# Kernel tuning notes

Measured on AMD Instinct MI355X. Metric: run time of the kernel, lower is better.

Reference implementation:

```python
import jax, jax.numpy as jnp
import numpy as np

N = 50000
D = 128
C = 40
E = 600000


def gcn_conv(x, src, dst, W, b, n):
    # PyG GCNConv: h = x @ W^T; symmetric deg^-1/2 normalization over
    # edges (self-loops already appended in src/dst); bias added after agg.
    h = x @ W.T                                   # [N, D_out]
    deg = jnp.zeros((n,), h.dtype).at[dst].add(jnp.ones((src.shape[0],), h.dtype))
    dinv = jnp.where(deg > 0, jax.lax.rsqrt(deg), 0.0)
    norm = dinv[src] * dinv[dst]                  # [E+N]
    msg = h[src] * norm[:, None]                  # gather + scale
    out = jnp.zeros_like(h).at[dst].add(msg)      # scatter-add aggregation
    return out + b


def setup_inputs() -> dict:
    key = jax.random.key(0)
    ks = jax.random.split(key, 8)
    x = jax.random.normal(ks[0], (N, D), dtype=jnp.float32)
    edge_index = jax.random.randint(ks[1], (2, E), 0, N, dtype=jnp.int64)
    s = 1.0 / np.sqrt(D)
    W1 = jax.random.uniform(ks[2], (D, D), jnp.float32, -s, s)
    b1 = jnp.zeros((D,), jnp.float32)
    W2 = jax.random.uniform(ks[3], (D, D), jnp.float32, -s, s)
    b2 = jnp.zeros((D,), jnp.float32)
    Wl = jax.random.uniform(ks[4], (C, D), jnp.float32, -s, s)
    bl = jnp.zeros((C,), jnp.float32)
    return {"x": x, "edge_index": edge_index, "W1": W1, "b1": b1,
            "W2": W2, "b2": b2, "Wl": Wl, "bl": bl}


def reference(x, edge_index, W1, b1, W2, b2, Wl, bl):
    n = x.shape[0]
    loop = jnp.arange(n, dtype=edge_index.dtype)
    src = jnp.concatenate([edge_index[0], loop])  # add self-loops
    dst = jnp.concatenate([edge_index[1], loop])
    h = gcn_conv(x, src, dst, W1, b1, n)
    h = jax.nn.relu(h)  # dropout is identity in eval mode
    h = gcn_conv(h, src, dst, W2, b2, n)
    h = jax.nn.relu(h)
    logits = h @ Wl.T + bl
    return jax.nn.log_softmax(logits, axis=1)
```

## Files before the change

### kernel.cpp

```cpp
#include <hip/hip_runtime.h>
#include <math.h>

#define FD  128
#define CAP 64

static __device__ __forceinline__ float4 ld4(const float* p){ return *(const float4*)p; }


__global__ __launch_bounds__(256) void k_fill(const int* __restrict__ src, const int* __restrict__ dst,
                                              int* __restrict__ cnt, int* __restrict__ bcol, int e){
    int i = blockIdx.x*blockDim.x + threadIdx.x;
    if (i < e){
        int s = src[i], d = dst[i];
        int pos = atomicAdd(&cnt[d], 1);
        if (pos < CAP) bcol[d*CAP + pos] = s;
    }
}


__global__ __launch_bounds__(256, 2) void k_gemm(const float* __restrict__ A, const float* __restrict__ W,
                                                 float* __restrict__ out, int nrows,
                                                 int* __restrict__ zcnt, int zn)
{
    __shared__ float Wt[128*128];
    __shared__ float xs[32*128];
    const int tid  = threadIdx.x;
    const int row0 = blockIdx.x * 32;

    int gid = blockIdx.x*256 + tid;
    if (zcnt && gid < zn) zcnt[gid] = 0;

    #pragma unroll
    for (int it = 0; it < 16; ++it){
        int idx4 = it*256 + tid;
        int j  = idx4 & 127;
        int k0 = (idx4 >> 7) << 2;
        float4 w = ld4(W + j*FD + k0);
        int jg = j >> 2, je = j & 3;
        Wt[(k0+0)*128 + (((jg + 2*(k0+0)) & 31) << 2) + je] = w.x;
        Wt[(k0+1)*128 + (((jg + 2*(k0+1)) & 31) << 2) + je] = w.y;
        Wt[(k0+2)*128 + (((jg + 2*(k0+2)) & 31) << 2) + je] = w.z;
        Wt[(k0+3)*128 + (((jg + 2*(k0+3)) & 31) << 2) + je] = w.w;
    }
    #pragma unroll
    for (int it = 0; it < 4; ++it){
        int idx4 = it*256 + tid;
        int r  = idx4 >> 5;
        int kq = idx4 & 31;
        int row = row0 + r;
        float4 v = make_float4(0.f,0.f,0.f,0.f);
        if (row < nrows) v = ld4(A + (size_t)row*FD + kq*4);
        *(float4*)&xs[r*128 + (((kq + r) & 31) << 2)] = v;
    }
    __syncthreads();

    const int tr = tid >> 4;
    const int tc = tid & 15;
    float acc[2][2][4];
    #pragma unroll
    for (int i = 0; i < 2; ++i)
        #pragma unroll
        for (int hh = 0; hh < 2; ++hh)
            #pragma unroll
            for (int u = 0; u < 4; ++u) acc[i][hh][u] = 0.f;

    #pragma unroll 4
    for (int k0 = 0; k0 < 128; k0 += 4){
        int kq = k0 >> 2;
        float4 a0 = *(const float4*)&xs[(2*tr+0)*128 + (((kq + 2*tr+0) & 31) << 2)];
        float4 a1 = *(const float4*)&xs[(2*tr+1)*128 + (((kq + 2*tr+1) & 31) << 2)];
        #pragma unroll
        for (int kk = 0; kk < 4; ++kk){
            int k = k0 + kk;
            float4 w0 = *(const float4*)&Wt[k*128 + (((tc      + 2*k) & 31) << 2)];
            float4 w1 = *(const float4*)&Wt[k*128 + (((tc + 16 + 2*k) & 31) << 2)];
            float av0 = (kk==0)?a0.x:(kk==1)?a0.y:(kk==2)?a0.z:a0.w;
            float av1 = (kk==0)?a1.x:(kk==1)?a1.y:(kk==2)?a1.z:a1.w;
            acc[0][0][0] += av0*w0.x; acc[0][0][1] += av0*w0.y; acc[0][0][2] += av0*w0.z; acc[0][0][3] += av0*w0.w;
            acc[0][1][0] += av0*w1.x; acc[0][1][1] += av0*w1.y; acc[0][1][2] += av0*w1.z; acc[0][1][3] += av0*w1.w;
            acc[1][0][0] += av1*w0.x; acc[1][0][1] += av1*w0.y; acc[1][0][2] += av1*w0.z; acc[1][0][3] += av1*w0.w;
            acc[1][1][0] += av1*w1.x; acc[1][1][1] += av1*w1.y; acc[1][1][2] += av1*w1.z; acc[1][1][3] += av1*w1.w;
        }
    }

    #pragma unroll
    for (int i = 0; i < 2; ++i){
        int row = row0 + 2*tr + i;
        if (row < nrows){
            *(float4*)(out + (size_t)row*FD + 4*tc)      = make_float4(acc[i][0][0],acc[i][0][1],acc[i][0][2],acc[i][0][3]);
            *(float4*)(out + (size_t)row*FD + 64 + 4*tc) = make_float4(acc[i][1][0],acc[i][1][1],acc[i][1][2],acc[i][1][3]);
        }
    }
}


__global__ __launch_bounds__(256) void k_agg(const float* __restrict__ t, const float* __restrict__ bias,
    const int* __restrict__ cnt, const int* __restrict__ bcol,
    float* __restrict__ out, int n, int relu)
{
    int node = (blockIdx.x*blockDim.x + threadIdx.x) >> 6;
    int lane = threadIdx.x & 63;
    if (node >= n) return;

    float2 b   = *(const float2*)(bias + lane*2);
    int deg = cnt[node];
    int dg  = min(deg, CAP);
    float dv = rsqrtf((float)(deg + 1));

    int   c_l = 0; float w_l = 0.f;
    if (lane < dg){
        c_l = bcol[node*CAP + lane];
        w_l = dv * rsqrtf((float)(cnt[c_l] + 1));
    }

    float2 acc = *(const float2*)(t + (size_t)node*FD + lane*2);
    float sw = dv*dv;
    acc.x = acc.x*sw + b.x;
    acc.y = acc.y*sw + b.y;

    int e = 0;
    for (; e + 4 <= dg; e += 4){
        int   c0 = __shfl(c_l, e,   64), c1 = __shfl(c_l, e+1, 64);
        int   c2 = __shfl(c_l, e+2, 64), c3 = __shfl(c_l, e+3, 64);
        float w0 = __shfl(w_l, e,   64), w1 = __shfl(w_l, e+1, 64);
        float w2 = __shfl(w_l, e+2, 64), w3 = __shfl(w_l, e+3, 64);
        float2 u0 = *(const float2*)(t + (size_t)c0*FD + lane*2);
        float2 u1 = *(const float2*)(t + (size_t)c1*FD + lane*2);
        float2 u2 = *(const float2*)(t + (size_t)c2*FD + lane*2);
        float2 u3 = *(const float2*)(t + (size_t)c3*FD + lane*2);
        acc.x += w0*u0.x + w1*u1.x + w2*u2.x + w3*u3.x;
        acc.y += w0*u0.y + w1*u1.y + w2*u2.y + w3*u3.y;
    }
    for (; e < dg; ++e){
        int   c = __shfl(c_l, e, 64);
        float w = __shfl(w_l, e, 64);
        float2 u = *(const float2*)(t + (size_t)c*FD + lane*2);
        acc.x += w*u.x; acc.y += w*u.y;
    }

    if (relu){ acc.x = fmaxf(acc.x, 0.f); acc.y = fmaxf(acc.y, 0.f); }
    *(float2*)(out + (size_t)node*FD + lane*2) = acc;
}


__global__ __launch_bounds__(320) void k_final(const float* __restrict__ h, const float* __restrict__ Wl,
    const float* __restrict__ bl, float* __restrict__ out, int n)
{
    __shared__ float Wt[128*41];
    __shared__ float xs[64*128];
    __shared__ float lg[64*41];
    const int tid  = threadIdx.x;
    const int row0 = blockIdx.x * 64;

    for (int idx4 = tid; idx4 < 1280; idx4 += 320){
        int j  = idx4 >> 5;
        int k0 = (idx4 & 31) << 2;
        float4 w = ld4(Wl + j*FD + k0);
        Wt[(k0+0)*41 + j] = w.x;
        Wt[(k0+1)*41 + j] = w.y;
        Wt[(k0+2)*41 + j] = w.z;
        Wt[(k0+3)*41 + j] = w.w;
    }
    for (int idx4 = tid; idx4 < 2048; idx4 += 320){
        int r = idx4 >> 5, kq = idx4 & 31;
        int row = row0 + r;
        float4 v = make_float4(0.f,0.f,0.f,0.f);
        if (row < n) v = ld4(h + (size_t)row*FD + kq*4);
        *(float4*)&xs[r*128 + kq*4] = v;
    }
    __syncthreads();

    const int c  = tid % 40;
    const int rb = tid / 40;
    float acc[8];
    #pragma unroll
    for (int i = 0; i < 8; ++i) acc[i] = 0.f;
    #pragma unroll 4
    for (int k = 0; k < 128; ++k){
        float w = Wt[k*41 + c];
        #pragma unroll
        for (int i = 0; i < 8; ++i) acc[i] += xs[(rb*8+i)*128 + k] * w;
    }
    float bv = bl[c];
    #pragma unroll
    for (int i = 0; i < 8; ++i) lg[(rb*8+i)*41 + c] = acc[i] + bv;
    __syncthreads();

    if (tid < 64){
        int row = row0 + tid;
        if (row < n){
            float v[40];
            #pragma unroll
            for (int j = 0; j < 40; ++j) v[j] = lg[tid*41 + j];
            float m = v[0];
            #pragma unroll
            for (int j = 1; j < 40; ++j) m = fmaxf(m, v[j]);
            float s = 0.f;
            #pragma unroll
            for (int j = 0; j < 40; ++j) s += expf(v[j] - m);
            float lse = m + logf(s);
            float* o = out + (size_t)row*40;
            #pragma unroll
            for (int j4 = 0; j4 < 10; ++j4){
                *(float4*)(o + 4*j4) = make_float4(v[4*j4+0]-lse, v[4*j4+1]-lse,
                                                   v[4*j4+2]-lse, v[4*j4+3]-lse);
            }
        }
    }
}


extern "C" void kernel_launch(void* const* d_in, const int* in_sizes, int n_in,
                              void* d_out, int out_size, void* d_ws, size_t ws_size,
                              hipStream_t stream)
{
    const float* x   = (const float*)d_in[0];
    const int*   ei  = (const int*)d_in[1];
    const float* W1  = (const float*)d_in[2];
    const float* b1  = (const float*)d_in[3];
    const float* W2  = (const float*)d_in[4];
    const float* b2  = (const float*)d_in[5];
    const float* Wl  = (const float*)d_in[6];
    const float* bl  = (const float*)d_in[7];
    float*       out = (float*)d_out;

    const int n = in_sizes[0] / FD;
    const int e = in_sizes[1] / 2;
    const int* src = ei;
    const int* dst = ei + e;

    char* p = (char*)d_ws;
    auto alloc = [&](size_t bytes)->char* {
        char* q = p; p += (bytes + 255) & ~(size_t)255; return q;
    };
    int*   cnt  = (int*)  alloc((size_t)n*4);
    int*   bcol = (int*)  alloc((size_t)n*CAP*4);
    float* t    = (float*)alloc((size_t)n*FD*4);
    float* h    = (float*)alloc((size_t)n*FD*4);

    const int gemm_grid  = (n + 31)/32;
    const int agg_grid   = (n + 3)/4;
    const int fill_grid  = (e + 255)/256;
    const int final_grid = (n + 63)/64;

    hipLaunchKernelGGL(k_gemm, dim3(gemm_grid), dim3(256), 0, stream, x, W1, t, n, cnt, n);
    hipLaunchKernelGGL(k_fill, dim3(fill_grid), dim3(256), 0, stream, src, dst, cnt, bcol, e);
    hipLaunchKernelGGL(k_agg,  dim3(agg_grid),  dim3(256), 0, stream, t, b1, cnt, bcol, h, n, 1);
    hipLaunchKernelGGL(k_gemm, dim3(gemm_grid), dim3(256), 0, stream, h, W2, t, n, (int*)nullptr, 0);
    hipLaunchKernelGGL(k_agg,  dim3(agg_grid),  dim3(256), 0, stream, t, b2, cnt, bcol, h, n, 1);
    hipLaunchKernelGGL(k_final, dim3(final_grid), dim3(320), 0, stream, h, Wl, bl, out, n);
}
```

Measured before the change: 329.7 us.

## Replace FP32 SIMT GEMM with split-bf16 MFMA GEMM and precomputed weight halves

Replaces the shared-memory FP32 FMA GEMM with a per-wave MFMA kernel using 16x16x32 bf16 instructions. Fp32 accuracy is approximated by splitting activations and weights into high and low bf16 parts and accumulating three products. A new prologue kernel converts W1/W2 to bf16 hi/lo arrays and zeroes the degree counters, which the old GEMM used to do. Weights are now read straight from global/L2 per wave rather than staged in LDS, and the output is written as scalar strided stores, which may cost memory efficiency; precision is slightly reduced versus pure fp32.

```diff
diff --git a/kernel.cpp b/kernel.cpp
--- a/kernel.cpp
+++ b/kernel.cpp
@@ -4,7 +4,39 @@
 #define FD  128
 #define CAP 64
 
+
 static __device__ __forceinline__ float4 ld4(const float* p){ return *(const float4*)p; }
+
+typedef __attribute__((ext_vector_type(8))) short bf16x8;
+typedef __attribute__((ext_vector_type(4))) float f32x4;
+
+static __device__ __forceinline__ unsigned short f2bf(float f){
+    union { float f; unsigned u; } c; c.f = f;
+    unsigned u = c.u + 0x7fffu + ((c.u >> 16) & 1u);
+    return (unsigned short)(u >> 16);
+}
+static __device__ __forceinline__ float bf2f(unsigned short b){
+    union { float f; unsigned u; } c; c.u = ((unsigned)b) << 16;
+    return c.f;
+}
+
+
+__global__ __launch_bounds__(256) void k_wconv(const float* __restrict__ W1, const float* __restrict__ W2,
+                                               unsigned short* __restrict__ w1h, unsigned short* __restrict__ w1l,
+                                               unsigned short* __restrict__ w2h, unsigned short* __restrict__ w2l,
+                                               int* __restrict__ cnt, int n)
+{
+    int i = blockIdx.x*256 + threadIdx.x;
+    if (i < n) cnt[i] = 0;
+    if (i < FD*FD){
+        float a = W1[i];
+        unsigned short ah = f2bf(a);
+        w1h[i] = ah; w1l[i] = f2bf(a - bf2f(ah));
+        float b = W2[i];
+        unsigned short bh = f2bf(b);
+        w2h[i] = bh; w2l[i] = f2bf(b - bf2f(bh));
+    }
+}
 
 
 __global__ __launch_bounds__(256) void k_fill(const int* __restrict__ src, const int* __restrict__ dst,
@@ -18,77 +50,64 @@
 }
 
 
-__global__ __launch_bounds__(256, 2) void k_gemm(const float* __restrict__ A, const float* __restrict__ W,
-                                                 float* __restrict__ out, int nrows,
-                                                 int* __restrict__ zcnt, int zn)
-{
-    __shared__ float Wt[128*128];
-    __shared__ float xs[32*128];
-    const int tid  = threadIdx.x;
-    const int row0 = blockIdx.x * 32;
-
-    int gid = blockIdx.x*256 + tid;
-    if (zcnt && gid < zn) zcnt[gid] = 0;
-
-    #pragma unroll
-    for (int it = 0; it < 16; ++it){
-        int idx4 = it*256 + tid;
-        int j  = idx4 & 127;
-        int k0 = (idx4 >> 7) << 2;
-        float4 w = ld4(W + j*FD + k0);
-        int jg = j >> 2, je = j & 3;
-        Wt[(k0+0)*128 + (((jg + 2*(k0+0)) & 31) << 2) + je] = w.x;
-        Wt[(k0+1)*128 + (((jg + 2*(k0+1)) & 31) << 2) + je] = w.y;
-        Wt[(k0+2)*128 + (((jg + 2*(k0+2)) & 31) << 2) + je] = w.z;
-        Wt[(k0+3)*128 + (((jg + 2*(k0+3)) & 31) << 2) + je] = w.w;
-    }
-    #pragma unroll
-    for (int it = 0; it < 4; ++it){
-        int idx4 = it*256 + tid;
-        int r  = idx4 >> 5;
-        int kq = idx4 & 31;
-        int row = row0 + r;
-        float4 v = make_float4(0.f,0.f,0.f,0.f);
-        if (row < nrows) v = ld4(A + (size_t)row*FD + kq*4);
-        *(float4*)&xs[r*128 + (((kq + r) & 31) << 2)] = v;
-    }
-    __syncthreads();
-
-    const int tr = tid >> 4;
-    const int tc = tid & 15;
-    float acc[2][2][4];
-    #pragma unroll
-    for (int i = 0; i < 2; ++i)
+__global__ __launch_bounds__(256) void k_gemm_mfma(const float* __restrict__ A,
+                                                   const unsigned short* __restrict__ Wh,
+                                                   const unsigned short* __restrict__ Wl,
+                                                   float* __restrict__ out, int nrows)
+{
+    const int lane = threadIdx.x & 63;
+    const int wid  = (blockIdx.x*blockDim.x + threadIdx.x) >> 6;
+    const int i0   = wid * 16;
+    if (i0 >= nrows) return;
+
+    const int mr = lane & 15;
+    const int kg = lane >> 4;
+
+    int arow = i0 + mr;
+    if (arow >= nrows) arow = nrows - 1;
+    const float* ap = A + (size_t)arow*FD + kg*8;
+
+    bf16x8 ahf[4], alf[4];
+    #pragma unroll
+    for (int kt = 0; kt < 4; ++kt){
+        float4 a0 = ld4(ap + 32*kt);
+        float4 a1 = ld4(ap + 32*kt + 4);
+        float v0 = a0.x, v1 = a0.y, v2 = a0.z, v3 = a0.w;
+        float v4 = a1.x, v5 = a1.y, v6 = a1.z, v7 = a1.w;
+        unsigned short h0=f2bf(v0),h1=f2bf(v1),h2=f2bf(v2),h3=f2bf(v3);
+        unsigned short h4=f2bf(v4),h5=f2bf(v5),h6=f2bf(v6),h7=f2bf(v7);
+        ahf[kt][0]=(short)h0; ahf[kt][1]=(short)h1; ahf[kt][2]=(short)h2; ahf[kt][3]=(short)h3;
+        ahf[kt][4]=(short)h4; ahf[kt][5]=(short)h5; ahf[kt][6]=(short)h6; ahf[kt][7]=(short)h7;
+        alf[kt][0]=(short)f2bf(v0-bf2f(h0)); alf[kt][1]=(short)f2bf(v1-bf2f(h1));
+        alf[kt][2]=(short)f2bf(v2-bf2f(h2)); alf[kt][3]=(short)f2bf(v3-bf2f(h3));
+        alf[kt][4]=(short)f2bf(v4-bf2f(h4)); alf[kt][5]=(short)f2bf(v5-bf2f(h5));
+        alf[kt][6]=(short)f2bf(v6-bf2f(h6)); alf[kt][7]=(short)f2bf(v7-bf2f(h7));
+    }
+
+    f32x4 acc[8];
+    #pragma unroll
+    for (int jt = 0; jt < 8; ++jt){ acc[jt][0]=0.f; acc[jt][1]=0.f; acc[jt][2]=0.f; acc[jt][3]=0.f; }
+
+    #pragma unroll
+    for (int kt = 0; kt < 4; ++kt){
         #pragma unroll
-        for (int hh = 0; hh < 2; ++hh)
-            #pragma unroll
-            for (int u = 0; u < 4; ++u) acc[i][hh][u] = 0.f;
-
-    #pragma unroll 4
-    for (int k0 = 0; k0 < 128; k0 += 4){
-        int kq = k0 >> 2;
-        float4 a0 = *(const float4*)&xs[(2*tr+0)*128 + (((kq + 2*tr+0) & 31) << 2)];
-        float4 a1 = *(const float4*)&xs[(2*tr+1)*128 + (((kq + 2*tr+1) & 31) << 2)];
-        #pragma unroll
-        for (int kk = 0; kk < 4; ++kk){
-            int k = k0 + kk;
-            float4 w0 = *(const float4*)&Wt[k*128 + (((tc      + 2*k) & 31) << 2)];
-            float4 w1 = *(const float4*)&Wt[k*128 + (((tc + 16 + 2*k) & 31) << 2)];
-            float av0 = (kk==0)?a0.x:(kk==1)?a0.y:(kk==2)?a0.z:a0.w;
-            float av1 = (kk==0)?a1.x:(kk==1)?a1.y:(kk==2)?a1.z:a1.w;
-            acc[0][0][0] += av0*w0.x; acc[0][0][1] += av0*w0.y; acc[0][0][2] += av0*w0.z; acc[0][0][3] += av0*w0.w;
-            acc[0][1][0] += av0*w1.x; acc[0][1][1] += av0*w1.y; acc[0][1][2] += av0*w1.z; acc[0][1][3] += av0*w1.w;
-            acc[1][0][0] += av1*w0.x; acc[1][0][1] += av1*w0.y; acc[1][0][2] += av1*w0.z; acc[1][0][3] += av1*w0.w;
-            acc[1][1][0] += av1*w1.x; acc[1][1][1] += av1*w1.y; acc[1][1][2] += av1*w1.z; acc[1][1][3] += av1*w1.w;
+        for (int jt = 0; jt < 8; ++jt){
+            size_t off = (size_t)(16*jt + mr)*FD + 32*kt + 8*kg;
+            bf16x8 wh = *(const bf16x8*)(Wh + off);
+            bf16x8 wl = *(const bf16x8*)(Wl + off);
+            acc[jt] = __builtin_amdgcn_mfma_f32_16x16x32_bf16(ahf[kt], wh, acc[jt], 0, 0, 0);
+            acc[jt] = __builtin_amdgcn_mfma_f32_16x16x32_bf16(ahf[kt], wl, acc[jt], 0, 0, 0);
+            acc[jt] = __builtin_amdgcn_mfma_f32_16x16x32_bf16(alf[kt], wh, acc[jt], 0, 0, 0);
         }
     }
 
     #pragma unroll
-    for (int i = 0; i < 2; ++i){
-        int row = row0 + 2*tr + i;
-        if (row < nrows){
-            *(float4*)(out + (size_t)row*FD + 4*tc)      = make_float4(acc[i][0][0],acc[i][0][1],acc[i][0][2],acc[i][0][3]);
-            *(float4*)(out + (size_t)row*FD + 64 + 4*tc) = make_float4(acc[i][1][0],acc[i][1][1],acc[i][1][2],acc[i][1][3]);
+    for (int r = 0; r < 4; ++r){
+        int orow = i0 + kg*4 + r;
+        if (orow < nrows){
+            float* op = out + (size_t)orow*FD + mr;
+            #pragma unroll
+            for (int jt = 0; jt < 8; ++jt) op[16*jt] = acc[jt][r];
         }
     }
 }
@@ -233,20 +252,29 @@
     auto alloc = [&](size_t bytes)->char* {
         char* q = p; p += (bytes + 255) & ~(size_t)255; return q;
     };
-    int*   cnt  = (int*)  alloc((size_t)n*4);
-    int*   bcol = (int*)  alloc((size_t)n*CAP*4);
-    float* t    = (float*)alloc((size_t)n*FD*4);
-    float* h    = (float*)alloc((size_t)n*FD*4);
-
-    const int gemm_grid  = (n + 31)/32;
+    int*            cnt  = (int*)           alloc((size_t)n*4);
+    int*            bcol = (int*)           alloc((size_t)n*CAP*4);
+    float*          t    = (float*)         alloc((size_t)n*FD*4);
+    float*          h    = (float*)         alloc((size_t)n*FD*4);
+    unsigned short* w1h  = (unsigned short*)alloc((size_t)FD*FD*2);
+    unsigned short* w1l  = (unsigned short*)alloc((size_t)FD*FD*2);
+    unsigned short* w2h  = (unsigned short*)alloc((size_t)FD*FD*2);
+    unsigned short* w2l  = (unsigned short*)alloc((size_t)FD*FD*2);
+
+    const int strips     = (n + 15)/16;
+    const int gemm_grid  = (strips + 3)/4;
     const int agg_grid   = (n + 3)/4;
     const int fill_grid  = (e + 255)/256;
     const int final_grid = (n + 63)/64;
-
-    hipLaunchKernelGGL(k_gemm, dim3(gemm_grid), dim3(256), 0, stream, x, W1, t, n, cnt, n);
+    const int conv_n     = (n > FD*FD) ? n : FD*FD;
+    const int conv_grid  = (conv_n + 255)/256;
+
+    hipLaunchKernelGGL(k_wconv, dim3(conv_grid), dim3(256), 0, stream,
+                       W1, W2, w1h, w1l, w2h, w2l, cnt, n);
     hipLaunchKernelGGL(k_fill, dim3(fill_grid), dim3(256), 0, stream, src, dst, cnt, bcol, e);
+    hipLaunchKernelGGL(k_gemm_mfma, dim3(gemm_grid), dim3(256), 0, stream, x, w1h, w1l, t, n);
     hipLaunchKernelGGL(k_agg,  dim3(agg_grid),  dim3(256), 0, stream, t, b1, cnt, bcol, h, n, 1);
-    hipLaunchKernelGGL(k_gemm, dim3(gemm_grid), dim3(256), 0, stream, h, W2, t, n, (int*)nullptr, 0);
+    hipLaunchKernelGGL(k_gemm_mfma, dim3(gemm_grid), dim3(256), 0, stream, h, w2h, w2l, t, n);
     hipLaunchKernelGGL(k_agg,  dim3(agg_grid),  dim3(256), 0, stream, t, b2, cnt, bcol, h, n, 1);
     hipLaunchKernelGGL(k_final, dim3(final_grid), dim3(320), 0, stream, h, Wl, bl, out, n);
 }
```

Result: faster. 316.8 us (-3.9%).
